# Performance work log

Measured on AMD Instinct MI355X. Metric: run time of the kernel, lower is better.

Reference implementation:

```python
import jax, jax.numpy as jnp
import numpy as np

TEMPERATURE = 0.9  # DiversityLoss temperature
EPS = 1e-6


def setup_inputs() -> dict:
    key = jax.random.key(0)
    kx, ke = jax.random.split(key)
    x = jax.random.normal(kx, (8, 4096, 128), dtype=jnp.float32)
    embed = jax.random.normal(ke, (2048, 128), dtype=jnp.float32)  # [codebook_size, dim]
    return {"x": x, "embed": embed}


def reference(x, embed):
    """EuclideanCodebook.forward (ema_update=True, eval mode: no buffer updates).

    Returns (quantize, embed_ind, diversity_loss).
    """
    shape = x.shape
    xf = x.reshape(-1, shape[-1])                       # [N, d]
    x_sq = jnp.sum(xf * xf, axis=1, keepdims=True)      # [N, 1]
    e_sq = jnp.sum(embed * embed, axis=1)[None, :]      # [1, K]
    confidence = -(x_sq - 2.0 * (xf @ embed.T) + e_sq)  # [N, K]
    embed_ind_flat = jnp.argmax(confidence, axis=-1)    # [N]
    # dequantize: gather codebook rows, restore leading shape
    quantize = jnp.take(embed, embed_ind_flat, axis=0).reshape(shape)
    embed_ind = embed_ind_flat.reshape(shape[:-1])
    # diversity loss: softmax over codes per point, mean over points, entropy-style sum
    point_probs = jax.nn.softmax(confidence / TEMPERATURE, axis=1)  # [N, K]
    class_probs = jnp.mean(point_probs, axis=0)                      # [K]
    diversity_loss = jnp.sum(class_probs * jnp.log(class_probs + EPS))
    return quantize, embed_ind, diversity_loss
```

## Files before the change

kernel.cpp:

```cpp
#include <hip/hip_runtime.h>
#include <math.h>

#define D        128
#define KCODES   2048
#define NPTS     32768
#define AS       136
#define INV_T    (1.0f / 0.9f)
#define LO_SCALE 4096.0f
#define LO_INV   (1.0f / 4096.0f)
#define CHUNK    64
#define NCHUNK   8
#define PSLICES  64
#define CSLICES  8

typedef _Float16 half8 __attribute__((ext_vector_type(8)));
typedef _Float16 half4 __attribute__((ext_vector_type(4)));
typedef float    f32x4 __attribute__((ext_vector_type(4)));

__global__ void prep_kernel(const float* __restrict__ embed,
                            float* __restrict__ e_sq,
                            _Float16* __restrict__ e_hi,
                            _Float16* __restrict__ e_lo,
                            float* __restrict__ classacc) {
    const int c = blockIdx.x;
    const int t = threadIdx.x;
    float v0 = embed[(size_t)c * D + t];
    float v1 = embed[(size_t)c * D + 64 + t];
    _Float16 h0 = (_Float16)v0;
    _Float16 h1 = (_Float16)v1;
    e_hi[(size_t)c * D + t]      = h0;
    e_hi[(size_t)c * D + 64 + t] = h1;
    e_lo[(size_t)c * D + t]      = (_Float16)((v0 - (float)h0) * LO_SCALE);
    e_lo[(size_t)c * D + 64 + t] = (_Float16)((v1 - (float)h1) * LO_SCALE);
    float s = v0 * v0 + v1 * v1;
    #pragma unroll
    for (int off = 32; off > 0; off >>= 1) s += __shfl_down(s, off, 64);
    if (t == 0) {
        e_sq[c] = s;
        classacc[c] = 0.0f;
    }
}

__device__ __forceinline__ void stage_x(const float4* __restrict__ x4,
                                        _Float16* ahi, _Float16* alo,
                                        int pbase, int tid) {
    #pragma unroll
    for (int it = 0; it < 8; ++it) {
        int j = tid + it * 256;
        int row = j >> 5;
        int d4 = j & 31;
        float4 v = x4[(size_t)(pbase + row) * 32 + d4];
        half4 h, l4;
        h.x = (_Float16)v.x; h.y = (_Float16)v.y;
        h.z = (_Float16)v.z; h.w = (_Float16)v.w;
        l4.x = (_Float16)((v.x - (float)h.x) * LO_SCALE);
        l4.y = (_Float16)((v.y - (float)h.y) * LO_SCALE);
        l4.z = (_Float16)((v.z - (float)h.z) * LO_SCALE);
        l4.w = (_Float16)((v.w - (float)h.w) * LO_SCALE);
        *(half4*)&ahi[row * AS + d4 * 4] = h;
        *(half4*)&alo[row * AS + d4 * 4] = l4;
    }
}

__global__ __launch_bounds__(256, 2)
void sweepA_kernel(const float* __restrict__ x,
                   const _Float16* __restrict__ e_hi_g,
                   const _Float16* __restrict__ e_lo_g,
                   const float* __restrict__ e_sq_g,
                   float* __restrict__ pm, float* __restrict__ pl,
                   int* __restrict__ pidx) {
    __shared__ _Float16 ahi[CHUNK * AS];
    __shared__ _Float16 alo[CHUNK * AS];
    __shared__ float cm[4][CHUNK];
    __shared__ float cl[4][CHUNK];
    __shared__ int   ci[4][CHUNK];

    const int tid  = threadIdx.x;
    const int w    = tid >> 6;
    const int lane = tid & 63;
    const int col  = lane & 15;
    const int quad = lane >> 4;
    const int cslice = blockIdx.y;
    const int pbase0 = blockIdx.x * (CHUNK * NCHUNK);
    const int c0w = cslice * 256 + w * 64;

    half8 bhi[4][4], blo[4][4];
    float esq_r[4];
    #pragma unroll
    for (int ct = 0; ct < 4; ++ct) {
        esq_r[ct] = e_sq_g[c0w + 16 * ct + col];
        #pragma unroll
        for (int kk = 0; kk < 4; ++kk) {
            size_t off = (size_t)(c0w + 16 * ct + col) * D + kk * 32 + quad * 8;
            bhi[ct][kk] = *(const half8*)(e_hi_g + off);
            blo[ct][kk] = *(const half8*)(e_lo_g + off);
        }
    }

    const float4* x4 = (const float4*)x;

    for (int chunk = 0; chunk < NCHUNK; ++chunk) {
        const int pbase = pbase0 + chunk * CHUNK;
        __syncthreads();
        stage_x(x4, ahi, alo, pbase, tid);
        __syncthreads();

        #pragma unroll
        for (int p = 0; p < 4; ++p) {
            half8 Ahi[4], Alo[4];
            #pragma unroll
            for (int kk = 0; kk < 4; ++kk) {
                int off = (16 * p + col) * AS + kk * 32 + quad * 8;
                Ahi[kk] = *(const half8*)&ahi[off];
                Alo[kk] = *(const half8*)&alo[off];
            }
            f32x4 chh[4], cx[4];
            #pragma unroll
            for (int ct = 0; ct < 4; ++ct) { chh[ct] = (f32x4){0,0,0,0}; cx[ct] = (f32x4){0,0,0,0}; }
            #pragma unroll
            for (int kk = 0; kk < 4; ++kk) {
                #pragma unroll
                for (int ct = 0; ct < 4; ++ct) {
                    chh[ct] = __builtin_amdgcn_mfma_f32_16x16x32_f16(Ahi[kk], bhi[ct][kk], chh[ct], 0, 0, 0);
                    cx[ct]  = __builtin_amdgcn_mfma_f32_16x16x32_f16(Ahi[kk], blo[ct][kk], cx[ct], 0, 0, 0);
                    cx[ct]  = __builtin_amdgcn_mfma_f32_16x16x32_f16(Alo[kk], bhi[ct][kk], cx[ct], 0, 0, 0);
                }
            }
            float lp[4] = {0.f, 0.f, 0.f, 0.f};
            float bv[4] = {-INFINITY, -INFINITY, -INFINITY, -INFINITY};
            int   bi[4] = {0, 0, 0, 0};
            #pragma unroll
            for (int ct = 0; ct < 4; ++ct) {
                int code = c0w + 16 * ct + col;
                #pragma unroll
                for (int r = 0; r < 4; ++r) {
                    float s = 2.0f * (chh[ct][r] + cx[ct][r] * LO_INV) - esq_r[ct];
                    lp[r] += __expf(s * INV_T);
                    if (s > bv[r]) { bv[r] = s; bi[r] = code; }
                }
            }
            #pragma unroll
            for (int r = 0; r < 4; ++r) {
                float v = bv[r]; int idx = bi[r]; float l = lp[r];
                #pragma unroll
                for (int off = 8; off >= 1; off >>= 1) {
                    float ov = __shfl_xor(v, off, 16);
                    int   oi = __shfl_xor(idx, off, 16);
                    float ol = __shfl_xor(l, off, 16);
                    l += ol;
                    if (ov > v || (ov == v && oi < idx)) { v = ov; idx = oi; }
                }
                if (col == 0) {
                    int row = p * 16 + quad * 4 + r;
                    cm[w][row] = v; cl[w][row] = l; ci[w][row] = idx;
                }
            }
        }
        __syncthreads();
        if (tid < CHUNK) {
            float bm = cm[0][tid]; int bidx = ci[0][tid]; float l = cl[0][tid];
            #pragma unroll
            for (int ww = 1; ww < 4; ++ww) {
                float v = cm[ww][tid]; int idx = ci[ww][tid];
                l += cl[ww][tid];
                if (v > bm) { bm = v; bidx = idx; }
            }
            size_t o = (size_t)cslice * NPTS + pbase + tid;
            pm[o] = bm; pl[o] = l; pidx[o] = bidx;
        }
    }
}

__global__ void combine_kernel(const float* __restrict__ pm, const float* __restrict__ pl,
                               const int* __restrict__ pidx,
                               float* __restrict__ r_buf, int* __restrict__ idx_buf,
                               float* __restrict__ ind_out) {
    const int p = blockIdx.x * 256 + threadIdx.x;
    float bm = -INFINITY; int bi = 0; float l = 0.0f;
    #pragma unroll
    for (int sl = 0; sl < CSLICES; ++sl) {
        size_t o = (size_t)sl * NPTS + p;
        float v = pm[o];
        l += pl[o];
        if (v > bm) { bm = v; bi = pidx[o]; }
    }
    r_buf[p] = 1.0f / l;
    idx_buf[p] = bi;
    ind_out[p] = (float)bi;
}

__global__ __launch_bounds__(256, 2)
void sweepB_kernel(const float* __restrict__ x,
                   const _Float16* __restrict__ e_hi_g,
                   const _Float16* __restrict__ e_lo_g,
                   const float* __restrict__ e_sq_g,
                   const float* __restrict__ r_buf,
                   float* __restrict__ classacc) {
    __shared__ _Float16 ahi[CHUNK * AS];
    __shared__ _Float16 alo[CHUNK * AS];
    __shared__ float r_s[CHUNK];

    const int tid  = threadIdx.x;
    const int w    = tid >> 6;
    const int lane = tid & 63;
    const int col  = lane & 15;
    const int quad = lane >> 4;
    const int cslice = blockIdx.y;
    const int pbase0 = blockIdx.x * (CHUNK * NCHUNK);
    const int c0w = cslice * 256 + w * 64;

    half8 bhi[4][4], blo[4][4];
    float esq_r[4];
    #pragma unroll
    for (int ct = 0; ct < 4; ++ct) {
        esq_r[ct] = e_sq_g[c0w + 16 * ct + col];
        #pragma unroll
        for (int kk = 0; kk < 4; ++kk) {
            size_t off = (size_t)(c0w + 16 * ct + col) * D + kk * 32 + quad * 8;
            bhi[ct][kk] = *(const half8*)(e_hi_g + off);
            blo[ct][kk] = *(const half8*)(e_lo_g + off);
        }
    }

    const float4* x4 = (const float4*)x;
    float csum[4] = {0.f, 0.f, 0.f, 0.f};

    for (int chunk = 0; chunk < NCHUNK; ++chunk) {
        const int pbase = pbase0 + chunk * CHUNK;
        __syncthreads();
        stage_x(x4, ahi, alo, pbase, tid);
        if (tid < CHUNK) r_s[tid] = r_buf[pbase + tid];
        __syncthreads();

        #pragma unroll
        for (int p = 0; p < 4; ++p) {
            half8 Ahi[4], Alo[4];
            #pragma unroll
            for (int kk = 0; kk < 4; ++kk) {
                int off = (16 * p + col) * AS + kk * 32 + quad * 8;
                Ahi[kk] = *(const half8*)&ahi[off];
                Alo[kk] = *(const half8*)&alo[off];
            }
            f32x4 chh[4], cx[4];
            #pragma unroll
            for (int ct = 0; ct < 4; ++ct) { chh[ct] = (f32x4){0,0,0,0}; cx[ct] = (f32x4){0,0,0,0}; }
            #pragma unroll
            for (int kk = 0; kk < 4; ++kk) {
                #pragma unroll
                for (int ct = 0; ct < 4; ++ct) {
                    chh[ct] = __builtin_amdgcn_mfma_f32_16x16x32_f16(Ahi[kk], bhi[ct][kk], chh[ct], 0, 0, 0);
                    cx[ct]  = __builtin_amdgcn_mfma_f32_16x16x32_f16(Ahi[kk], blo[ct][kk], cx[ct], 0, 0, 0);
                    cx[ct]  = __builtin_amdgcn_mfma_f32_16x16x32_f16(Alo[kk], bhi[ct][kk], cx[ct], 0, 0, 0);
                }
            }
            float rr[4];
            #pragma unroll
            for (int r = 0; r < 4; ++r) rr[r] = r_s[p * 16 + quad * 4 + r];
            #pragma unroll
            for (int ct = 0; ct < 4; ++ct) {
                #pragma unroll
                for (int r = 0; r < 4; ++r) {
                    float s = 2.0f * (chh[ct][r] + cx[ct][r] * LO_INV) - esq_r[ct];
                    csum[ct] += __expf(s * INV_T) * rr[r];
                }
            }
        }
    }

    #pragma unroll
    for (int ct = 0; ct < 4; ++ct) {
        float v = csum[ct];
        v += __shfl_xor(v, 16, 64);
        v += __shfl_xor(v, 32, 64);
        if (quad == 0) atomicAdd(&classacc[c0w + 16 * ct + col], v);
    }
}

__global__ void gather_kernel(const float* __restrict__ embed,
                              const int* __restrict__ idx_buf,
                              float* __restrict__ q_out) {
    const int j = blockIdx.x * 256 + threadIdx.x;
    const int row = j >> 5;
    const int d4 = j & 31;
    reinterpret_cast<float4*>(q_out)[(size_t)row * 32 + d4] =
        reinterpret_cast<const float4*>(embed)[(size_t)idx_buf[row] * 32 + d4];
}

__global__ void finalize_kernel(const float* __restrict__ classacc,
                                float* __restrict__ loss_out, int N, int K) {
    __shared__ float red[256];
    const int tid = threadIdx.x;
    float s = 0.0f;
    const float invN = 1.0f / (float)N;
    for (int i = tid; i < K; i += 256) {
        float cp = classacc[i] * invN;
        s += cp * logf(cp + 1e-6f);
    }
    red[tid] = s;
    __syncthreads();
    for (int off = 128; off > 0; off >>= 1) {
        if (tid < off) red[tid] += red[tid + off];
        __syncthreads();
    }
    if (tid == 0) loss_out[0] = red[0];
}

extern "C" void kernel_launch(void* const* d_in, const int* in_sizes, int n_in,
                              void* d_out, int out_size, void* d_ws, size_t ws_size,
                              hipStream_t stream) {
    const float* x     = (const float*)d_in[0];
    const float* embed = (const float*)d_in[1];

    float* out      = (float*)d_out;
    float* q_out    = out;
    float* ind_out  = out + (size_t)NPTS * D;
    float* loss_out = ind_out + NPTS;

    float*    e_sq  = (float*)d_ws;
    float*    cacc  = e_sq + KCODES;
    _Float16* e_hi  = (_Float16*)(cacc + KCODES);
    _Float16* e_lo  = e_hi + (size_t)KCODES * D;
    float*    pm    = (float*)(e_lo + (size_t)KCODES * D);
    float*    pl    = pm + (size_t)CSLICES * NPTS;
    int*      pidx  = (int*)(pl + (size_t)CSLICES * NPTS);
    float*    r_buf = (float*)(pidx + (size_t)CSLICES * NPTS);
    int*      idx_buf = (int*)(r_buf + NPTS);

    dim3 sgrid(PSLICES, CSLICES);

    prep_kernel<<<KCODES, 64, 0, stream>>>(embed, e_sq, e_hi, e_lo, cacc);
    sweepA_kernel<<<sgrid, 256, 0, stream>>>(x, e_hi, e_lo, e_sq, pm, pl, pidx);
    combine_kernel<<<NPTS / 256, 256, 0, stream>>>(pm, pl, pidx, r_buf, idx_buf, ind_out);
    sweepB_kernel<<<sgrid, 256, 0, stream>>>(x, e_hi, e_lo, e_sq, r_buf, cacc);
    gather_kernel<<<NPTS * 32 / 256, 256, 0, stream>>>(embed, idx_buf, q_out);
    finalize_kernel<<<1, 256, 0, stream>>>(cacc, loss_out, NPTS, KCODES);
}
```

Baseline: 225.5 us.

## Swap operand roles: keep points in registers, stream codebook tiles via LDS

Both sweep kernels now hold each wave's 64 points (hi/lo fp16 split) in registers and stream 64-code tiles of the pre-split codebook through shared memory. Previously the codebook slice sat in registers and x was converted and staged per chunk. The grid changes to 128x4 blocks covering 512 codes each. The score math is folded into base-2 constants so the exp becomes exp2f and the esq scale is precomputed. Sweep B accumulates per-code sums in LDS bins before one global atomic per code. This removes repeated fp32-to-fp16 conversion of x and the per-chunk cross-wave reduction, at the cost of more per-thread register state and LDS atomics.

```diff
diff --git a/kernel.cpp b/kernel.cpp
--- a/kernel.cpp
+++ b/kernel.cpp
@@ -5,20 +5,21 @@
 #define KCODES   2048
 #define NPTS     32768
 #define AS       136
-#define INV_T    (1.0f / 0.9f)
 #define LO_SCALE 4096.0f
-#define LO_INV   (1.0f / 4096.0f)
+#define CSLICES  4
+#define CODES_PER_SLICE 512
 #define CHUNK    64
-#define NCHUNK   8
-#define PSLICES  64
-#define CSLICES  8
+#define NCHUNK   (CODES_PER_SLICE / CHUNK)
+#define PSLICES  (NPTS / 256)
+#define C1       3.205988979753252f
+#define C2       (C1 / LO_SCALE)
+#define ESQ_SCALE 1.602994489876626f
 
 typedef _Float16 half8 __attribute__((ext_vector_type(8)));
-typedef _Float16 half4 __attribute__((ext_vector_type(4)));
 typedef float    f32x4 __attribute__((ext_vector_type(4)));
 
 __global__ void prep_kernel(const float* __restrict__ embed,
-                            float* __restrict__ e_sq,
+                            float* __restrict__ e_sqt,
                             _Float16* __restrict__ e_hi,
                             _Float16* __restrict__ e_lo,
                             float* __restrict__ classacc) {
@@ -36,29 +37,43 @@
     #pragma unroll
     for (int off = 32; off > 0; off >>= 1) s += __shfl_down(s, off, 64);
     if (t == 0) {
-        e_sq[c] = s;
+        e_sqt[c] = s * ESQ_SCALE;
         classacc[c] = 0.0f;
     }
 }
 
-__device__ __forceinline__ void stage_x(const float4* __restrict__ x4,
-                                        _Float16* ahi, _Float16* alo,
-                                        int pbase, int tid) {
-    #pragma unroll
-    for (int it = 0; it < 8; ++it) {
-        int j = tid + it * 256;
-        int row = j >> 5;
-        int d4 = j & 31;
-        float4 v = x4[(size_t)(pbase + row) * 32 + d4];
-        half4 h, l4;
-        h.x = (_Float16)v.x; h.y = (_Float16)v.y;
-        h.z = (_Float16)v.z; h.w = (_Float16)v.w;
-        l4.x = (_Float16)((v.x - (float)h.x) * LO_SCALE);
-        l4.y = (_Float16)((v.y - (float)h.y) * LO_SCALE);
-        l4.z = (_Float16)((v.z - (float)h.z) * LO_SCALE);
-        l4.w = (_Float16)((v.w - (float)h.w) * LO_SCALE);
-        *(half4*)&ahi[row * AS + d4 * 4] = h;
-        *(half4*)&alo[row * AS + d4 * 4] = l4;
+__device__ __forceinline__ void stage_e(const uint4* __restrict__ ehi_g4,
+                                        const uint4* __restrict__ elo_g4,
+                                        _Float16* ehi, _Float16* elo,
+                                        int cbase, int tid) {
+    #pragma unroll
+    for (int it = 0; it < 4; ++it) {
+        int j   = tid + it * 256;
+        int row = j >> 4;
+        int c8  = j & 15;
+        uint4 vh = ehi_g4[(size_t)cbase * 16 + j];
+        uint4 vl = elo_g4[(size_t)cbase * 16 + j];
+        *(uint4*)&ehi[row * AS + c8 * 8] = vh;
+        *(uint4*)&elo[row * AS + c8 * 8] = vl;
+    }
+}
+
+__device__ __forceinline__ void load_a(const float* __restrict__ x,
+                                       int p0w, int col, int quad,
+                                       half8 ahi[4][4], half8 alo[4][4]) {
+    #pragma unroll
+    for (int pt = 0; pt < 4; ++pt) {
+        const float* xp = x + (size_t)(p0w + pt * 16 + col) * D + quad * 8;
+        #pragma unroll
+        for (int kk = 0; kk < 4; ++kk) {
+            #pragma unroll
+            for (int j = 0; j < 8; ++j) {
+                float v = xp[kk * 32 + j];
+                _Float16 h = (_Float16)v;
+                ahi[pt][kk][j] = h;
+                alo[pt][kk][j] = (_Float16)((v - (float)h) * LO_SCALE);
+            }
+        }
     }
 }
 
@@ -66,14 +81,12 @@
 void sweepA_kernel(const float* __restrict__ x,
                    const _Float16* __restrict__ e_hi_g,
                    const _Float16* __restrict__ e_lo_g,
-                   const float* __restrict__ e_sq_g,
+                   const float* __restrict__ e_sqt_g,
                    float* __restrict__ pm, float* __restrict__ pl,
                    int* __restrict__ pidx) {
-    __shared__ _Float16 ahi[CHUNK * AS];
-    __shared__ _Float16 alo[CHUNK * AS];
-    __shared__ float cm[4][CHUNK];
-    __shared__ float cl[4][CHUNK];
-    __shared__ int   ci[4][CHUNK];
+    __shared__ _Float16 ehi[CHUNK * AS];
+    __shared__ _Float16 elo[CHUNK * AS];
+    __shared__ float esq_s[CODES_PER_SLICE];
 
     const int tid  = threadIdx.x;
     const int w    = tid >> 6;
@@ -81,92 +94,79 @@
     const int col  = lane & 15;
     const int quad = lane >> 4;
     const int cslice = blockIdx.y;
-    const int pbase0 = blockIdx.x * (CHUNK * NCHUNK);
-    const int c0w = cslice * 256 + w * 64;
-
-    half8 bhi[4][4], blo[4][4];
-    float esq_r[4];
-    #pragma unroll
-    for (int ct = 0; ct < 4; ++ct) {
-        esq_r[ct] = e_sq_g[c0w + 16 * ct + col];
-        #pragma unroll
-        for (int kk = 0; kk < 4; ++kk) {
-            size_t off = (size_t)(c0w + 16 * ct + col) * D + kk * 32 + quad * 8;
-            bhi[ct][kk] = *(const half8*)(e_hi_g + off);
-            blo[ct][kk] = *(const half8*)(e_lo_g + off);
-        }
-    }
-
-    const float4* x4 = (const float4*)x;
+    const int c0   = cslice * CODES_PER_SLICE;
+    const int p0w  = blockIdx.x * 256 + w * 64;
+
+    for (int i = tid; i < CODES_PER_SLICE; i += 256) esq_s[i] = e_sqt_g[c0 + i];
+
+    half8 ahi[4][4], alo[4][4];
+    load_a(x, p0w, col, quad, ahi, alo);
+
+    const uint4* ehi_g4 = (const uint4*)e_hi_g;
+    const uint4* elo_g4 = (const uint4*)e_lo_g;
+
+    float lrun[4][4], bv[4][4];
+    int   bi[4][4];
+    #pragma unroll
+    for (int pt = 0; pt < 4; ++pt)
+        #pragma unroll
+        for (int r = 0; r < 4; ++r) { lrun[pt][r] = 0.f; bv[pt][r] = -INFINITY; bi[pt][r] = 0; }
 
     for (int chunk = 0; chunk < NCHUNK; ++chunk) {
-        const int pbase = pbase0 + chunk * CHUNK;
-        __syncthreads();
-        stage_x(x4, ahi, alo, pbase, tid);
-        __syncthreads();
-
-        #pragma unroll
-        for (int p = 0; p < 4; ++p) {
-            half8 Ahi[4], Alo[4];
+        const int cbase = c0 + chunk * CHUNK;
+        __syncthreads();
+        stage_e(ehi_g4, elo_g4, ehi, elo, cbase, tid);
+        __syncthreads();
+
+        #pragma unroll
+        for (int ct = 0; ct < 4; ++ct) {
+            f32x4 chh[4], cx[4];
+            #pragma unroll
+            for (int pt = 0; pt < 4; ++pt) { chh[pt] = (f32x4){0,0,0,0}; cx[pt] = (f32x4){0,0,0,0}; }
             #pragma unroll
             for (int kk = 0; kk < 4; ++kk) {
-                int off = (16 * p + col) * AS + kk * 32 + quad * 8;
-                Ahi[kk] = *(const half8*)&ahi[off];
-                Alo[kk] = *(const half8*)&alo[off];
-            }
-            f32x4 chh[4], cx[4];
-            #pragma unroll
-            for (int ct = 0; ct < 4; ++ct) { chh[ct] = (f32x4){0,0,0,0}; cx[ct] = (f32x4){0,0,0,0}; }
-            #pragma unroll
-            for (int kk = 0; kk < 4; ++kk) {
+                const int boff = (ct * 16 + col) * AS + kk * 32 + quad * 8;
+                half8 Bhi = *(const half8*)&ehi[boff];
+                half8 Blo = *(const half8*)&elo[boff];
                 #pragma unroll
-                for (int ct = 0; ct < 4; ++ct) {
-                    chh[ct] = __builtin_amdgcn_mfma_f32_16x16x32_f16(Ahi[kk], bhi[ct][kk], chh[ct], 0, 0, 0);
-                    cx[ct]  = __builtin_amdgcn_mfma_f32_16x16x32_f16(Ahi[kk], blo[ct][kk], cx[ct], 0, 0, 0);
-                    cx[ct]  = __builtin_amdgcn_mfma_f32_16x16x32_f16(Alo[kk], bhi[ct][kk], cx[ct], 0, 0, 0);
+                for (int pt = 0; pt < 4; ++pt) {
+                    chh[pt] = __builtin_amdgcn_mfma_f32_16x16x32_f16(ahi[pt][kk], Bhi, chh[pt], 0, 0, 0);
+                    cx[pt]  = __builtin_amdgcn_mfma_f32_16x16x32_f16(ahi[pt][kk], Blo, cx[pt], 0, 0, 0);
+                    cx[pt]  = __builtin_amdgcn_mfma_f32_16x16x32_f16(alo[pt][kk], Bhi, cx[pt], 0, 0, 0);
                 }
             }
-            float lp[4] = {0.f, 0.f, 0.f, 0.f};
-            float bv[4] = {-INFINITY, -INFINITY, -INFINITY, -INFINITY};
-            int   bi[4] = {0, 0, 0, 0};
-            #pragma unroll
-            for (int ct = 0; ct < 4; ++ct) {
-                int code = c0w + 16 * ct + col;
+            const int code = chunk * CHUNK + ct * 16 + col;
+            const float esqT = esq_s[code];
+            const int gcode = c0 + code;
+            #pragma unroll
+            for (int pt = 0; pt < 4; ++pt) {
                 #pragma unroll
                 for (int r = 0; r < 4; ++r) {
-                    float s = 2.0f * (chh[ct][r] + cx[ct][r] * LO_INV) - esq_r[ct];
-                    lp[r] += __expf(s * INV_T);
-                    if (s > bv[r]) { bv[r] = s; bi[r] = code; }
+                    float s2 = fmaf(chh[pt][r], C1, fmaf(cx[pt][r], C2, -esqT));
+                    lrun[pt][r] += exp2f(s2);
+                    if (s2 > bv[pt][r]) { bv[pt][r] = s2; bi[pt][r] = gcode; }
                 }
             }
-            #pragma unroll
-            for (int r = 0; r < 4; ++r) {
-                float v = bv[r]; int idx = bi[r]; float l = lp[r];
-                #pragma unroll
-                for (int off = 8; off >= 1; off >>= 1) {
-                    float ov = __shfl_xor(v, off, 16);
-                    int   oi = __shfl_xor(idx, off, 16);
-                    float ol = __shfl_xor(l, off, 16);
-                    l += ol;
-                    if (ov > v || (ov == v && oi < idx)) { v = ov; idx = oi; }
-                }
-                if (col == 0) {
-                    int row = p * 16 + quad * 4 + r;
-                    cm[w][row] = v; cl[w][row] = l; ci[w][row] = idx;
-                }
-            }
         }
-        __syncthreads();
-        if (tid < CHUNK) {
-            float bm = cm[0][tid]; int bidx = ci[0][tid]; float l = cl[0][tid];
-            #pragma unroll
-            for (int ww = 1; ww < 4; ++ww) {
-                float v = cm[ww][tid]; int idx = ci[ww][tid];
-                l += cl[ww][tid];
-                if (v > bm) { bm = v; bidx = idx; }
-            }
-            size_t o = (size_t)cslice * NPTS + pbase + tid;
-            pm[o] = bm; pl[o] = l; pidx[o] = bidx;
+    }
+
+    #pragma unroll
+    for (int pt = 0; pt < 4; ++pt) {
+        #pragma unroll
+        for (int r = 0; r < 4; ++r) {
+            float v = bv[pt][r]; int idx = bi[pt][r]; float l = lrun[pt][r];
+            #pragma unroll
+            for (int off = 8; off >= 1; off >>= 1) {
+                float ov = __shfl_xor(v, off, 16);
+                int   oi = __shfl_xor(idx, off, 16);
+                float ol = __shfl_xor(l, off, 16);
+                l += ol;
+                if (ov > v || (ov == v && oi < idx)) { v = ov; idx = oi; }
+            }
+            if (col == 0) {
+                size_t o = (size_t)cslice * NPTS + p0w + pt * 16 + quad * 4 + r;
+                pm[o] = v; pl[o] = l; pidx[o] = idx;
+            }
         }
     }
 }
@@ -193,12 +193,13 @@
 void sweepB_kernel(const float* __restrict__ x,
                    const _Float16* __restrict__ e_hi_g,
                    const _Float16* __restrict__ e_lo_g,
-                   const float* __restrict__ e_sq_g,
+                   const float* __restrict__ e_sqt_g,
                    const float* __restrict__ r_buf,
                    float* __restrict__ classacc) {
-    __shared__ _Float16 ahi[CHUNK * AS];
-    __shared__ _Float16 alo[CHUNK * AS];
-    __shared__ float r_s[CHUNK];
+    __shared__ _Float16 ehi[CHUNK * AS];
+    __shared__ _Float16 elo[CHUNK * AS];
+    __shared__ float esq_s[CODES_PER_SLICE];
+    __shared__ float bins[CODES_PER_SLICE];
 
     const int tid  = threadIdx.x;
     const int w    = tid >> 6;
@@ -206,74 +207,70 @@
     const int col  = lane & 15;
     const int quad = lane >> 4;
     const int cslice = blockIdx.y;
-    const int pbase0 = blockIdx.x * (CHUNK * NCHUNK);
-    const int c0w = cslice * 256 + w * 64;
-
-    half8 bhi[4][4], blo[4][4];
-    float esq_r[4];
-    #pragma unroll
-    for (int ct = 0; ct < 4; ++ct) {
-        esq_r[ct] = e_sq_g[c0w + 16 * ct + col];
-        #pragma unroll
-        for (int kk = 0; kk < 4; ++kk) {
-            size_t off = (size_t)(c0w + 16 * ct + col) * D + kk * 32 + quad * 8;
-            bhi[ct][kk] = *(const half8*)(e_hi_g + off);
-            blo[ct][kk] = *(const half8*)(e_lo_g + off);
-        }
-    }
-
-    const float4* x4 = (const float4*)x;
-    float csum[4] = {0.f, 0.f, 0.f, 0.f};
+    const int c0   = cslice * CODES_PER_SLICE;
+    const int p0w  = blockIdx.x * 256 + w * 64;
+
+    for (int i = tid; i < CODES_PER_SLICE; i += 256) {
+        esq_s[i] = e_sqt_g[c0 + i];
+        bins[i] = 0.0f;
+    }
+
+    half8 ahi[4][4], alo[4][4];
+    load_a(x, p0w, col, quad, ahi, alo);
+
+    float rr[4][4];
+    #pragma unroll
+    for (int pt = 0; pt < 4; ++pt)
+        #pragma unroll
+        for (int r = 0; r < 4; ++r)
+            rr[pt][r] = r_buf[p0w + pt * 16 + quad * 4 + r];
+
+    const uint4* ehi_g4 = (const uint4*)e_hi_g;
+    const uint4* elo_g4 = (const uint4*)e_lo_g;
 
     for (int chunk = 0; chunk < NCHUNK; ++chunk) {
-        const int pbase = pbase0 + chunk * CHUNK;
-        __syncthreads();
-        stage_x(x4, ahi, alo, pbase, tid);
-        if (tid < CHUNK) r_s[tid] = r_buf[pbase + tid];
-        __syncthreads();
-
-        #pragma unroll
-        for (int p = 0; p < 4; ++p) {
-            half8 Ahi[4], Alo[4];
+        const int cbase = c0 + chunk * CHUNK;
+        __syncthreads();
+        stage_e(ehi_g4, elo_g4, ehi, elo, cbase, tid);
+        __syncthreads();
+
+        #pragma unroll
+        for (int ct = 0; ct < 4; ++ct) {
+            f32x4 chh[4], cx[4];
+            #pragma unroll
+            for (int pt = 0; pt < 4; ++pt) { chh[pt] = (f32x4){0,0,0,0}; cx[pt] = (f32x4){0,0,0,0}; }
             #pragma unroll
             for (int kk = 0; kk < 4; ++kk) {
-                int off = (16 * p + col) * AS + kk * 32 + quad * 8;
-                Ahi[kk] = *(const half8*)&ahi[off];
-                Alo[kk] = *(const half8*)&alo[off];
-            }
-            f32x4 chh[4], cx[4];
-            #pragma unroll
-            for (int ct = 0; ct < 4; ++ct) { chh[ct] = (f32x4){0,0,0,0}; cx[ct] = (f32x4){0,0,0,0}; }
-            #pragma unroll
-            for (int kk = 0; kk < 4; ++kk) {
+                const int boff = (ct * 16 + col) * AS + kk * 32 + quad * 8;
+                half8 Bhi = *(const half8*)&ehi[boff];
+                half8 Blo = *(const half8*)&elo[boff];
                 #pragma unroll
-                for (int ct = 0; ct < 4; ++ct) {
-                    chh[ct] = __builtin_amdgcn_mfma_f32_16x16x32_f16(Ahi[kk], bhi[ct][kk], chh[ct], 0, 0, 0);
-                    cx[ct]  = __builtin_amdgcn_mfma_f32_16x16x32_f16(Ahi[kk], blo[ct][kk], cx[ct], 0, 0, 0);
-                    cx[ct]  = __builtin_amdgcn_mfma_f32_16x16x32_f16(Alo[kk], bhi[ct][kk], cx[ct], 0, 0, 0);
+                for (int pt = 0; pt < 4; ++pt) {
+                    chh[pt] = __builtin_amdgcn_mfma_f32_16x16x32_f16(ahi[pt][kk], Bhi, chh[pt], 0, 0, 0);
+                    cx[pt]  = __builtin_amdgcn_mfma_f32_16x16x32_f16(ahi[pt][kk], Blo, cx[pt], 0, 0, 0);
+                    cx[pt]  = __builtin_amdgcn_mfma_f32_16x16x32_f16(alo[pt][kk], Bhi, cx[pt], 0, 0, 0);
                 }
             }
-            float rr[4];
-            #pragma unroll
-            for (int r = 0; r < 4; ++r) rr[r] = r_s[p * 16 + quad * 4 + r];
-            #pragma unroll
-            for (int ct = 0; ct < 4; ++ct) {
+            const int code = chunk * CHUNK + ct * 16 + col;
+            const float esqT = esq_s[code];
+            float wsum = 0.0f;
+            #pragma unroll
+            for (int pt = 0; pt < 4; ++pt) {
                 #pragma unroll
                 for (int r = 0; r < 4; ++r) {
-                    float s = 2.0f * (chh[ct][r] + cx[ct][r] * LO_INV) - esq_r[ct];
-                    csum[ct] += __expf(s * INV_T) * rr[r];
+                    float s2 = fmaf(chh[pt][r], C1, fmaf(cx[pt][r], C2, -esqT));
+                    wsum += exp2f(s2) * rr[pt][r];
                 }
             }
+            wsum += __shfl_xor(wsum, 16, 64);
+            wsum += __shfl_xor(wsum, 32, 64);
+            if (quad == 0) atomicAdd(&bins[code], wsum);
         }
     }
 
-    #pragma unroll
-    for (int ct = 0; ct < 4; ++ct) {
-        float v = csum[ct];
-        v += __shfl_xor(v, 16, 64);
-        v += __shfl_xor(v, 32, 64);
-        if (quad == 0) atomicAdd(&classacc[c0w + 16 * ct + col], v);
-    }
+    __syncthreads();
+    for (int i = tid; i < CODES_PER_SLICE; i += 256)
+        atomicAdd(&classacc[c0 + i], bins[i]);
 }
 
 __global__ void gather_kernel(const float* __restrict__ embed,
@@ -316,8 +313,8 @@
     float* ind_out  = out + (size_t)NPTS * D;
     float* loss_out = ind_out + NPTS;
 
-    float*    e_sq  = (float*)d_ws;
-    float*    cacc  = e_sq + KCODES;
+    float*    e_sqt = (float*)d_ws;
+    float*    cacc  = e_sqt + KCODES;
     _Float16* e_hi  = (_Float16*)(cacc + KCODES);
     _Float16* e_lo  = e_hi + (size_t)KCODES * D;
     float*    pm    = (float*)(e_lo + (size_t)KCODES * D);
@@ -328,10 +325,10 @@
 
     dim3 sgrid(PSLICES, CSLICES);
 
-    prep_kernel<<<KCODES, 64, 0, stream>>>(embed, e_sq, e_hi, e_lo, cacc);
-    sweepA_kernel<<<sgrid, 256, 0, stream>>>(x, e_hi, e_lo, e_sq, pm, pl, pidx);
+    prep_kernel<<<KCODES, 64, 0, stream>>>(embed, e_sqt, e_hi, e_lo, cacc);
+    sweepA_kernel<<<sgrid, 256, 0, stream>>>(x, e_hi, e_lo, e_sqt, pm, pl, pidx);
     combine_kernel<<<NPTS / 256, 256, 0, stream>>>(pm, pl, pidx, r_buf, idx_buf, ind_out);
-    sweepB_kernel<<<sgrid, 256, 0, stream>>>(x, e_hi, e_lo, e_sq, r_buf, cacc);
+    sweepB_kernel<<<sgrid, 256, 0, stream>>>(x, e_hi, e_lo, e_sqt, r_buf, cacc);
     gather_kernel<<<NPTS * 32 / 256, 256, 0, stream>>>(embed, idx_buf, q_out);
     finalize_kernel<<<1, 256, 0, stream>>>(cacc, loss_out, NPTS, KCODES);
 }
```

Result: slower. 285.0 us (+26.4%).
